# Optimization experiments

Measured on AMD Instinct MI355X. Metric: run time of the kernel, lower is better.

The kernel has to match this reference:

```python
import jax, jax.numpy as jnp
import numpy as np

NEG_SLOPE = 0.2  # PyG GATConv default negative_slope


def gat_conv(h_in, src, dst, W, a_src, a_dst, bias, concat):
    """PyG GATConv: linear -> per-edge attention -> segment softmax -> scatter-add.
    h_in: [N, Fin]; W: [heads*C, Fin]; a_src/a_dst: [heads, C]; bias: [heads*C] or [C].
    add_self_loops=True (PyG default)."""
    N = h_in.shape[0]
    heads, C = a_src.shape
    loop = jnp.arange(N, dtype=src.dtype)
    s = jnp.concatenate([src, loop])
    d = jnp.concatenate([dst, loop])
    h = (h_in @ W.T).reshape(N, heads, C)          # [N, H, C]
    al_s = (h * a_src).sum(-1)                      # [N, H]
    al_d = (h * a_dst).sum(-1)                      # [N, H]
    e = jax.nn.leaky_relu(al_s[s] + al_d[d], NEG_SLOPE)  # [E, H]
    emax = jax.ops.segment_max(e, d, num_segments=N)     # every node has a self loop
    ex = jnp.exp(e - emax[d])
    denom = jax.ops.segment_sum(ex, d, num_segments=N)
    alpha = ex / denom[d]                           # [E, H]
    msg = alpha[:, :, None] * h[s]                  # [E, H, C]
    out = jax.ops.segment_sum(msg, d, num_segments=N)    # [N, H, C]
    if concat:
        out = out.reshape(N, heads * C)
    else:
        out = out.mean(axis=1)
    return out + bias


def setup_inputs() -> dict:
    key = jax.random.key(0)
    ks = jax.random.split(key, 14)
    B, N, T = 1, 20000, 4
    E = 320000
    HID, HEADS, OUT = 64, 4, 64
    sc = 0.1
    x = jax.random.normal(ks[0], (B, N, T), dtype=jnp.float32)
    edge_index = jax.random.randint(ks[1], (2, E), 0, N, dtype=jnp.int64)
    time_idx = jnp.arange(T, dtype=jnp.float32).reshape(T, 1)
    return {
        "x": x,
        "edge_index": edge_index,
        "time_idx": time_idx,
        "Wt": jax.random.normal(ks[2], (HID, 1), jnp.float32) * sc,
        "bt": jnp.zeros((HID,), jnp.float32),
        "Wf": jax.random.normal(ks[3], (HID, 1), jnp.float32) * sc,
        "bf": jnp.zeros((HID,), jnp.float32),
        "W1": jax.random.normal(ks[4], (HEADS * HID, HID), jnp.float32) * sc,
        "a_src1": jax.random.normal(ks[5], (HEADS, HID), jnp.float32) * sc,
        "a_dst1": jax.random.normal(ks[6], (HEADS, HID), jnp.float32) * sc,
        "b1": jnp.zeros((HEADS * HID,), jnp.float32),
        "temporal_attention": jnp.ones((T,), jnp.float32),
        "W2": jax.random.normal(ks[7], (OUT, HEADS * HID), jnp.float32) * sc,
        "a_src2": jax.random.normal(ks[8], (1, OUT), jnp.float32) * sc,
        "a_dst2": jax.random.normal(ks[9], (1, OUT), jnp.float32) * sc,
        "b2": jnp.zeros((OUT,), jnp.float32),
    }


def reference(x, edge_index, time_idx, Wt, bt, Wf, bf, W1, a_src1, a_dst1, b1,
              temporal_attention, W2, a_src2, a_dst2, b2):
    B, N, T = x.shape  # features dim == time_steps
    src, dst = edge_index[0], edge_index[1]
    time_emb = time_idx @ Wt.T + bt                 # [T, hidden]
    tw = jax.nn.softmax(temporal_attention)         # [T]
    combined = jnp.zeros((B * N, a_src1.shape[0] * a_src1.shape[1]), x.dtype)
    for t in range(T):  # small static time loop, as in original
        feats = x[:, :, t].reshape(-1, 1)           # [B*N, 1]
        emb = feats @ Wf.T + bf + time_emb[t]       # [B*N, hidden]
        h = gat_conv(emb, src, dst, W1, a_src1, a_dst1, b1, concat=True)
        combined = combined + tw[t] * jax.nn.relu(h)  # dropout is identity in eval
    out = gat_conv(combined, src, dst, W2, a_src2, a_dst2, b2, concat=False)
    return out.reshape(B, N, -1)
```

## Files before the change

kernel.cpp:

```cpp
#include <hip/hip_runtime.h>
#include <hip/hip_bf16.h>

#define NEG 0.2f
#define NELL 64

#define P_U   0
#define P_W   256
#define P_PS  1280
#define P_PD  1284
#define P_QS  1288
#define P_QD  1304
#define P_TW  1320
#define P_WT  1324
#define P_CNT 2560

typedef __bf16 bf16x8 __attribute__((ext_vector_type(8)));
typedef float  f32x4  __attribute__((ext_vector_type(4)));

__device__ __forceinline__ float lrelu(float v){ return v > 0.f ? v : NEG*v; }
__device__ __forceinline__ unsigned short f2bf(float f){
    unsigned u = __float_as_uint(f);
    unsigned r = u + 0x7fffu + ((u >> 16) & 1u);
    return (unsigned short)(r >> 16);
}
__device__ __forceinline__ float bflo(unsigned u){ return __uint_as_float(u << 16); }
__device__ __forceinline__ float bfhi(unsigned u){ return __uint_as_float(u & 0xffff0000u); }

__global__ void zeroK(int* deg, int N){
    int i = blockIdx.x*256 + threadIdx.x;
    if (i < N) deg[i] = 0;
}

__global__ void ellpreK(const int* ei, int E, int* deg, int* ell,
                        const float* time_idx, const float* Wt, const float* bt,
                        const float* Wf, const float* bf, const float* W1,
                        const float* as1, const float* ad1, const float* b1,
                        const float* ta, const float* W2,
                        float* P, unsigned short* W2bf, int EB)
{
    int tid = threadIdx.x, bid = blockIdx.x;
    if (bid < EB){
        int e = bid*256 + tid;
        if (e < E){
            int d = ei[E+e];
            int pos = atomicAdd(&deg[d], 1);
            if (pos < NELL) ell[d*NELL + pos] = ei[e];
        }
        return;
    }
    if (bid > EB){
        int i0 = (bid - EB - 1)*256 + tid;
        for (int i = i0; i < 16384; i += 40*256) W2bf[i] = f2bf(W2[i]);
        return;
    }
    __shared__ float Zl[5][64];
    if (tid < 64){
        float wtk = Wt[tid], btk = bt[tid], bfk = bf[tid];
        Zl[0][tid] = Wf[tid];
        #pragma unroll
        for (int t = 0; t < 4; ++t)
            Zl[1+t][tid] = bfk + time_idx[t]*wtk + btk;
    }
    __syncthreads();
    {
        const float* wrow = W1 + tid*64;
        float uu = 0.f, v0 = 0.f, v1 = 0.f, v2 = 0.f, v3 = 0.f;
        for (int k = 0; k < 64; k += 4){
            float4 w4 = *reinterpret_cast<const float4*>(wrow + k);
            uu += w4.x*Zl[0][k] + w4.y*Zl[0][k+1] + w4.z*Zl[0][k+2] + w4.w*Zl[0][k+3];
            v0 += w4.x*Zl[1][k] + w4.y*Zl[1][k+1] + w4.z*Zl[1][k+2] + w4.w*Zl[1][k+3];
            v1 += w4.x*Zl[2][k] + w4.y*Zl[2][k+1] + w4.z*Zl[2][k+2] + w4.w*Zl[2][k+3];
            v2 += w4.x*Zl[3][k] + w4.y*Zl[3][k+1] + w4.z*Zl[3][k+2] + w4.w*Zl[3][k+3];
            v3 += w4.x*Zl[4][k] + w4.y*Zl[4][k+1] + w4.z*Zl[4][k+2] + w4.w*Zl[4][k+3];
        }
        float b = b1[tid];
        P[P_U + tid] = uu;
        P[P_W + 0*256 + tid] = v0 + b;
        P[P_W + 1*256 + tid] = v1 + b;
        P[P_W + 2*256 + tid] = v2 + b;
        P[P_W + 3*256 + tid] = v3 + b;
    }
    __syncthreads();
    if (tid < 4){
        int h = tid; float ps = 0.f, pd = 0.f;
        for (int c = 0; c < 64; ++c){
            float uv = P[P_U + h*64 + c];
            ps += uv * as1[h*64+c];
            pd += uv * ad1[h*64+c];
        }
        P[P_PS+h] = ps; P[P_PD+h] = pd;
    }
    if (tid < 16){
        int t = tid >> 2, h = tid & 3;
        float qs = 0.f, qd = 0.f;
        for (int c = 0; c < 64; ++c){
            float v = P[P_W + t*256 + h*64 + c] - b1[h*64+c];
            qs += v * as1[h*64+c];
            qd += v * ad1[h*64+c];
        }
        P[P_QS + t*4 + h] = qs;
        P[P_QD + t*4 + h] = qd;
    }
    if (tid == 0){
        float m = ta[0];
        for (int t = 1; t < 4; ++t) m = fmaxf(m, ta[t]);
        float s = 0.f, e[4];
        for (int t = 0; t < 4; ++t){ e[t] = __expf(ta[t]-m); s += e[t]; }
        for (int t = 0; t < 4; ++t) P[P_TW+t] = e[t]/s;
    }
    __syncthreads();
    for (int idx = tid; idx < 1024; idx += 256){
        int c = idx >> 2, t = idx & 3;
        P[P_WT + idx] = P[P_W + t*256 + c];
    }
}

__launch_bounds__(256)
__global__ void gat1h2K(const float* x, const int* deg, const int* ell,
                        const float* P, const unsigned short* W2bfg,
                        const float* as2, const float* ad2,
                        unsigned short* h2bf, float* als2, float* ald2, int N)
{
    __shared__ unsigned short Abf[64*264];
    __shared__ float4 Sl[64][4];
    __shared__ float  Ul[256];
    __shared__ float4 WTl[256];
    __shared__ float  Pl[44];
    int tid = threadIdx.x;
    Ul[tid] = P[P_U + tid];
    WTl[tid] = reinterpret_cast<const float4*>(P + P_WT)[tid];
    if (tid < 44) Pl[tid] = P[P_PS + tid];
    __syncthreads();

    int nl = tid >> 2, t = tid & 3;
    int n  = blockIdx.x*64 + nl;
    {
        float s_out[4] = {0.f,0.f,0.f,0.f};
        if (n < N){
            float xn = x[n*4 + t];
            float ps[4], qsum[4], den[4], num[4];
            #pragma unroll
            for (int h = 0; h < 4; ++h){
                ps[h]   = Pl[h];
                qsum[h] = Pl[8 + t*4 + h] + xn*Pl[4 + h] + Pl[24 + t*4 + h];
                float ex = __expf(lrelu(xn*ps[h] + qsum[h]));
                den[h] = ex; num[h] = ex*xn;
            }
            int dgn = min(deg[n], NELL);
            const int* row = ell + n*NELL;
            int j = 0;
            for (; j + 4 <= dgn; j += 4){
                float v0 = x[row[j]*4 + t];
                float v1 = x[row[j+1]*4 + t];
                float v2 = x[row[j+2]*4 + t];
                float v3 = x[row[j+3]*4 + t];
                #pragma unroll
                for (int h = 0; h < 4; ++h){
                    float e0 = __expf(lrelu(v0*ps[h] + qsum[h]));
                    float e1 = __expf(lrelu(v1*ps[h] + qsum[h]));
                    float e2 = __expf(lrelu(v2*ps[h] + qsum[h]));
                    float e3 = __expf(lrelu(v3*ps[h] + qsum[h]));
                    den[h] += (e0 + e1) + (e2 + e3);
                    num[h] += e0*v0 + e1*v1 + e2*v2 + e3*v3;
                }
            }
            for (; j < dgn; ++j){
                float v = x[row[j]*4 + t];
                #pragma unroll
                for (int h = 0; h < 4; ++h){
                    float ex = __expf(lrelu(v*ps[h] + qsum[h]));
                    den[h] += ex; num[h] += ex*v;
                }
            }
            #pragma unroll
            for (int h = 0; h < 4; ++h) s_out[h] = num[h]/den[h];
        }
        #pragma unroll
        for (int h = 0; h < 4; ++h)
            reinterpret_cast<float*>(&Sl[nl][h])[t] = s_out[h];
    }
    __syncthreads();

    {
        float tw0 = Pl[40], tw1 = Pl[41], tw2 = Pl[42], tw3 = Pl[43];
        int q = t;
        float4 s4 = Sl[nl][q];
        unsigned int* arow = reinterpret_cast<unsigned int*>(&Abf[nl*264 + q*64]);
        #pragma unroll 8
        for (int jj = 0; jj < 64; jj += 2){
            int c = q*64 + jj;
            float4 wa = WTl[c], wb = WTl[c+1];
            float ua = Ul[c], ub = Ul[c+1];
            float v0 = tw0*fmaxf(s4.x*ua + wa.x, 0.f) + tw1*fmaxf(s4.y*ua + wa.y, 0.f)
                     + tw2*fmaxf(s4.z*ua + wa.z, 0.f) + tw3*fmaxf(s4.w*ua + wa.w, 0.f);
            float v1 = tw0*fmaxf(s4.x*ub + wb.x, 0.f) + tw1*fmaxf(s4.y*ub + wb.y, 0.f)
                     + tw2*fmaxf(s4.z*ub + wb.z, 0.f) + tw3*fmaxf(s4.w*ub + wb.w, 0.f);
            arow[jj>>1] = (unsigned)f2bf(v0) | ((unsigned)f2bf(v1) << 16);
        }
    }
    __syncthreads();

    int w = tid >> 6, lane = tid & 63, lr = lane & 15, lhi = lane >> 4;
    int r0 = w*16;
    bf16x8 a[8];
    #pragma unroll
    for (int kk = 0; kk < 8; ++kk)
        a[kk] = *reinterpret_cast<const bf16x8*>(&Abf[(r0+lr)*264 + kk*32 + lhi*8]);
    float s1[4] = {0.f,0.f,0.f,0.f}, s2[4] = {0.f,0.f,0.f,0.f};
    int gbase = blockIdx.x*64 + r0 + lhi*4;
    #pragma unroll
    for (int nt = 0; nt < 4; ++nt){
        f32x4 acc = {0.f,0.f,0.f,0.f};
        const unsigned short* bp = W2bfg + (nt*16 + lr)*256 + lhi*8;
        #pragma unroll
        for (int kk = 0; kk < 8; ++kk){
            bf16x8 b = *reinterpret_cast<const bf16x8*>(bp + kk*32);
            acc = __builtin_amdgcn_mfma_f32_16x16x32_bf16(a[kk], b, acc, 0, 0, 0);
        }
        float oas = as2[nt*16 + lr], oad = ad2[nt*16 + lr];
        #pragma unroll
        for (int r = 0; r < 4; ++r){
            int g = gbase + r;
            if (g < N) h2bf[(size_t)g*64 + nt*16 + lr] = f2bf(acc[r]);
            s1[r] += acc[r]*oas;
            s2[r] += acc[r]*oad;
        }
    }
    #pragma unroll
    for (int r = 0; r < 4; ++r){
        float v1 = s1[r], v2 = s2[r];
        #pragma unroll
        for (int off = 8; off > 0; off >>= 1){
            v1 += __shfl_xor(v1, off);
            v2 += __shfl_xor(v2, off);
        }
        int g = gbase + r;
        if (lr == 0 && g < N){ als2[g] = v1; ald2[g] = v2; }
    }
}

__launch_bounds__(256)
__global__ void attnpvK(const unsigned short* h2bf, const float* als2, const float* ald2,
                        const int* deg, const int* ell, const float* b2,
                        float* out, int N)
{
    __shared__ int   sbuf[8][32];
    __shared__ float wbuf[8][32];
    int hw = threadIdx.x >> 5, lane = threadIdx.x & 31;
    int n = blockIdx.x*8 + hw;
    if (n >= N) return;
    float aldn = ald2[n];
    int dgn = min(deg[n], NELL);
    const int* row = ell + n*NELL;
    float sw = __expf(lrelu(als2[n] + aldn));
    float den = sw;
    unsigned us = reinterpret_cast<const unsigned*>(h2bf + ((size_t)n<<6))[lane];
    float acc0 = sw * bflo(us);
    float acc1 = sw * bfhi(us);
    for (int base = 0; base < dgn; base += 32){
        int cnt = min(32, dgn - base);
        int j = base + lane;
        int s = 0; float ex = 0.f;
        if (j < dgn){ s = row[j]; ex = __expf(lrelu(als2[s] + aldn)); }
        sbuf[hw][lane] = s; wbuf[hw][lane] = ex;
        float sx = ex;
        #pragma unroll
        for (int off = 16; off; off >>= 1) sx += __shfl_xor(sx, off);
        den += sx;
        int i = 0;
        for (; i + 4 <= cnt; i += 4){
            int   s0 = sbuf[hw][i],   s1 = sbuf[hw][i+1], s2 = sbuf[hw][i+2], s3 = sbuf[hw][i+3];
            float w0 = wbuf[hw][i],   w1 = wbuf[hw][i+1], w2 = wbuf[hw][i+2], w3 = wbuf[hw][i+3];
            unsigned g0 = reinterpret_cast<const unsigned*>(h2bf + ((size_t)s0<<6))[lane];
            unsigned g1 = reinterpret_cast<const unsigned*>(h2bf + ((size_t)s1<<6))[lane];
            unsigned g2 = reinterpret_cast<const unsigned*>(h2bf + ((size_t)s2<<6))[lane];
            unsigned g3 = reinterpret_cast<const unsigned*>(h2bf + ((size_t)s3<<6))[lane];
            acc0 += w0*bflo(g0); acc1 += w0*bfhi(g0);
            acc0 += w1*bflo(g1); acc1 += w1*bfhi(g1);
            acc0 += w2*bflo(g2); acc1 += w2*bfhi(g2);
            acc0 += w3*bflo(g3); acc1 += w3*bfhi(g3);
        }
        for (; i < cnt; ++i){
            float wv = wbuf[hw][i];
            unsigned g = reinterpret_cast<const unsigned*>(h2bf + ((size_t)sbuf[hw][i]<<6))[lane];
            acc0 += wv*bflo(g); acc1 += wv*bfhi(g);
        }
    }
    float rd = 1.f/den;
    int c = lane*2;
    float2 o;
    o.x = acc0*rd + b2[c];
    o.y = acc1*rd + b2[c+1];
    reinterpret_cast<float2*>(out + (size_t)n*64)[lane] = o;
}

extern "C" void kernel_launch(void* const* d_in, const int* in_sizes, int n_in,
                              void* d_out, int out_size, void* d_ws, size_t ws_size,
                              hipStream_t stream)
{
    const float* x        = (const float*)d_in[0];
    const int*   ei       = (const int*)  d_in[1];
    const float* time_idx = (const float*)d_in[2];
    const float* Wt       = (const float*)d_in[3];
    const float* bt       = (const float*)d_in[4];
    const float* Wf       = (const float*)d_in[5];
    const float* bf       = (const float*)d_in[6];
    const float* W1       = (const float*)d_in[7];
    const float* as1      = (const float*)d_in[8];
    const float* ad1      = (const float*)d_in[9];
    const float* b1       = (const float*)d_in[10];
    const float* ta       = (const float*)d_in[11];
    const float* W2       = (const float*)d_in[12];
    const float* as2      = (const float*)d_in[13];
    const float* ad2      = (const float*)d_in[14];
    const float* b2       = (const float*)d_in[15];

    int N = in_sizes[0] / 4;
    int E = in_sizes[1] / 2;

    char* w = (char*)d_ws;
    auto al = [](size_t v){ return (v + 255) & ~(size_t)255; };
    size_t off = 0;
    float* P     = (float*)(w + off); off = al(off + P_CNT*sizeof(float));
    unsigned short* W2bf = (unsigned short*)(w + off); off = al(off + 16384*sizeof(unsigned short));
    int*   deg   = (int*)  (w + off); off = al(off + (size_t)N*sizeof(int));
    int*   ell   = (int*)  (w + off); off = al(off + (size_t)N*NELL*sizeof(int));
    unsigned short* h2bf = (unsigned short*)(w + off); off = al(off + (size_t)N*64*sizeof(unsigned short));
    float* als2  = (float*)(w + off); off = al(off + (size_t)N*sizeof(float));
    float* ald2  = (float*)(w + off); off = al(off + (size_t)N*sizeof(float));
    (void)off; (void)ws_size; (void)n_in; (void)out_size;

    int EB = (E + 255)/256;

    zeroK<<<(N + 255)/256, 256, 0, stream>>>(deg, N);
    ellpreK<<<EB + 41, 256, 0, stream>>>(ei, E, deg, ell,
                                         time_idx, Wt, bt, Wf, bf, W1, as1, ad1, b1, ta, W2,
                                         P, W2bf, EB);
    gat1h2K<<<(N + 63)/64, 256, 0, stream>>>(x, deg, ell, P, W2bf, as2, ad2, h2bf, als2, ald2, N);
    attnpvK<<<(N + 7)/8, 256, 0, stream>>>(h2bf, als2, ald2, deg, ell, b2, (float*)d_out, N);
}
```

Measured before the change: 65.53 us.

## Halve nodes per block in gat1h2K, split edge loop across thread pairs

```diff
diff --git a/kernel.cpp b/kernel.cpp
--- a/kernel.cpp
+++ b/kernel.cpp
@@ -3,6 +3,7 @@
 
 #define NEG 0.2f
 #define NELL 64
+#define GT 32
 
 #define P_U   0
 #define P_W   256
@@ -121,21 +122,24 @@
                         const float* as2, const float* ad2,
                         unsigned short* h2bf, float* als2, float* ald2, int N)
 {
-    __shared__ unsigned short Abf[64*264];
-    __shared__ float4 Sl[64][4];
+    __shared__ unsigned short Abf[GT*264];
+    __shared__ float  Slf[GT][4][4];
     __shared__ float  Ul[256];
     __shared__ float4 WTl[256];
     __shared__ float  Pl[44];
+    __shared__ float  redL[2][2][GT];
     int tid = threadIdx.x;
     Ul[tid] = P[P_U + tid];
     WTl[tid] = reinterpret_cast<const float4*>(P + P_WT)[tid];
     if (tid < 44) Pl[tid] = P[P_PS + tid];
     __syncthreads();
 
-    int nl = tid >> 2, t = tid & 3;
-    int n  = blockIdx.x*64 + nl;
+    int nl = tid >> 3, sub = tid & 7, t = sub >> 1, half = sub & 1;
+    int n0 = blockIdx.x*GT;
+    int n  = n0 + nl;
+
     {
-        float s_out[4] = {0.f,0.f,0.f,0.f};
+        float o[4] = {0.f,0.f,0.f,0.f};
         if (n < N){
             float xn = x[n*4 + t];
             float ps[4], qsum[4], den[4], num[4];
@@ -143,17 +147,17 @@
             for (int h = 0; h < 4; ++h){
                 ps[h]   = Pl[h];
                 qsum[h] = Pl[8 + t*4 + h] + xn*Pl[4 + h] + Pl[24 + t*4 + h];
-                float ex = __expf(lrelu(xn*ps[h] + qsum[h]));
-                den[h] = ex; num[h] = ex*xn;
+                if (half == 0){
+                    float ex = __expf(lrelu(xn*ps[h] + qsum[h]));
+                    den[h] = ex; num[h] = ex*xn;
+                } else { den[h] = 0.f; num[h] = 0.f; }
             }
             int dgn = min(deg[n], NELL);
             const int* row = ell + n*NELL;
-            int j = 0;
-            for (; j + 4 <= dgn; j += 4){
-                float v0 = x[row[j]*4 + t];
-                float v1 = x[row[j+1]*4 + t];
-                float v2 = x[row[j+2]*4 + t];
-                float v3 = x[row[j+3]*4 + t];
+            int j = half;
+            for (; j + 6 < dgn; j += 8){
+                int s0 = row[j], s1 = row[j+2], s2 = row[j+4], s3 = row[j+6];
+                float v0 = x[s0*4 + t], v1 = x[s1*4 + t], v2 = x[s2*4 + t], v3 = x[s3*4 + t];
                 #pragma unroll
                 for (int h = 0; h < 4; ++h){
                     float e0 = __expf(lrelu(v0*ps[h] + qsum[h]));
@@ -164,7 +168,7 @@
                     num[h] += e0*v0 + e1*v1 + e2*v2 + e3*v3;
                 }
             }
-            for (; j < dgn; ++j){
+            for (; j < dgn; j += 2){
                 float v = x[row[j]*4 + t];
                 #pragma unroll
                 for (int h = 0; h < 4; ++h){
@@ -173,69 +177,85 @@
                 }
             }
             #pragma unroll
-            for (int h = 0; h < 4; ++h) s_out[h] = num[h]/den[h];
-        }
-        #pragma unroll
-        for (int h = 0; h < 4; ++h)
-            reinterpret_cast<float*>(&Sl[nl][h])[t] = s_out[h];
+            for (int h = 0; h < 4; ++h){
+                float d = den[h] + __shfl_xor(den[h], 1);
+                float m = num[h] + __shfl_xor(num[h], 1);
+                o[h] = m/d;
+            }
+        }
+        if (half == 0){
+            #pragma unroll
+            for (int h = 0; h < 4; ++h) Slf[nl][h][t] = o[h];
+        }
     }
     __syncthreads();
 
     {
+        int q = sub, h = q >> 1;
         float tw0 = Pl[40], tw1 = Pl[41], tw2 = Pl[42], tw3 = Pl[43];
-        int q = t;
-        float4 s4 = Sl[nl][q];
-        unsigned int* arow = reinterpret_cast<unsigned int*>(&Abf[nl*264 + q*64]);
+        float sx = Slf[nl][h][0], sy = Slf[nl][h][1], sz = Slf[nl][h][2], sw = Slf[nl][h][3];
+        unsigned* arow = reinterpret_cast<unsigned*>(&Abf[nl*264 + q*32]);
         #pragma unroll 8
-        for (int jj = 0; jj < 64; jj += 2){
-            int c = q*64 + jj;
+        for (int jj = 0; jj < 32; jj += 2){
+            int c = q*32 + jj;
             float4 wa = WTl[c], wb = WTl[c+1];
             float ua = Ul[c], ub = Ul[c+1];
-            float v0 = tw0*fmaxf(s4.x*ua + wa.x, 0.f) + tw1*fmaxf(s4.y*ua + wa.y, 0.f)
-                     + tw2*fmaxf(s4.z*ua + wa.z, 0.f) + tw3*fmaxf(s4.w*ua + wa.w, 0.f);
-            float v1 = tw0*fmaxf(s4.x*ub + wb.x, 0.f) + tw1*fmaxf(s4.y*ub + wb.y, 0.f)
-                     + tw2*fmaxf(s4.z*ub + wb.z, 0.f) + tw3*fmaxf(s4.w*ub + wb.w, 0.f);
+            float v0 = tw0*fmaxf(sx*ua + wa.x, 0.f) + tw1*fmaxf(sy*ua + wa.y, 0.f)
+                     + tw2*fmaxf(sz*ua + wa.z, 0.f) + tw3*fmaxf(sw*ua + wa.w, 0.f);
+            float v1 = tw0*fmaxf(sx*ub + wb.x, 0.f) + tw1*fmaxf(sy*ub + wb.y, 0.f)
+                     + tw2*fmaxf(sz*ub + wb.z, 0.f) + tw3*fmaxf(sw*ub + wb.w, 0.f);
             arow[jj>>1] = (unsigned)f2bf(v0) | ((unsigned)f2bf(v1) << 16);
         }
     }
     __syncthreads();
 
-    int w = tid >> 6, lane = tid & 63, lr = lane & 15, lhi = lane >> 4;
-    int r0 = w*16;
-    bf16x8 a[8];
-    #pragma unroll
-    for (int kk = 0; kk < 8; ++kk)
-        a[kk] = *reinterpret_cast<const bf16x8*>(&Abf[(r0+lr)*264 + kk*32 + lhi*8]);
-    float s1[4] = {0.f,0.f,0.f,0.f}, s2[4] = {0.f,0.f,0.f,0.f};
-    int gbase = blockIdx.x*64 + r0 + lhi*4;
-    #pragma unroll
-    for (int nt = 0; nt < 4; ++nt){
-        f32x4 acc = {0.f,0.f,0.f,0.f};
-        const unsigned short* bp = W2bfg + (nt*16 + lr)*256 + lhi*8;
-        #pragma unroll
-        for (int kk = 0; kk < 8; ++kk){
-            bf16x8 b = *reinterpret_cast<const bf16x8*>(bp + kk*32);
-            acc = __builtin_amdgcn_mfma_f32_16x16x32_bf16(a[kk], b, acc, 0, 0, 0);
-        }
-        float oas = as2[nt*16 + lr], oad = ad2[nt*16 + lr];
+    {
+        int w = tid >> 6, lane = tid & 63, lr = lane & 15, lhi = lane >> 4;
+        int rg = w & 1, cg = w >> 1;
+        bf16x8 a[8];
+        #pragma unroll
+        for (int kk = 0; kk < 8; ++kk)
+            a[kk] = *reinterpret_cast<const bf16x8*>(&Abf[(rg*16 + lr)*264 + kk*32 + lhi*8]);
+        float s1[4] = {0.f,0.f,0.f,0.f}, s2[4] = {0.f,0.f,0.f,0.f};
+        int gbase = n0 + rg*16 + lhi*4;
+        #pragma unroll
+        for (int nt2 = 0; nt2 < 2; ++nt2){
+            int nt = cg*2 + nt2;
+            f32x4 acc = {0.f,0.f,0.f,0.f};
+            const unsigned short* bp = W2bfg + (nt*16 + lr)*256 + lhi*8;
+            #pragma unroll
+            for (int kk = 0; kk < 8; ++kk){
+                bf16x8 b = *reinterpret_cast<const bf16x8*>(bp + kk*32);
+                acc = __builtin_amdgcn_mfma_f32_16x16x32_bf16(a[kk], b, acc, 0, 0, 0);
+            }
+            int o = nt*16 + lr;
+            float oas = as2[o], oad = ad2[o];
+            #pragma unroll
+            for (int r = 0; r < 4; ++r){
+                int g = gbase + r;
+                if (g < N) h2bf[(size_t)g*64 + o] = f2bf(acc[r]);
+                s1[r] += acc[r]*oas;
+                s2[r] += acc[r]*oad;
+            }
+        }
         #pragma unroll
         for (int r = 0; r < 4; ++r){
-            int g = gbase + r;
-            if (g < N) h2bf[(size_t)g*64 + nt*16 + lr] = f2bf(acc[r]);
-            s1[r] += acc[r]*oas;
-            s2[r] += acc[r]*oad;
-        }
-    }
-    #pragma unroll
-    for (int r = 0; r < 4; ++r){
-        float v1 = s1[r], v2 = s2[r];
-        #pragma unroll
-        for (int off = 8; off > 0; off >>= 1){
-            v1 += __shfl_xor(v1, off);
-            v2 += __shfl_xor(v2, off);
-        }
-        int g = gbase + r;
-        if (lr == 0 && g < N){ als2[g] = v1; ald2[g] = v2; }
+            float v1 = s1[r], v2 = s2[r];
+            #pragma unroll
+            for (int off = 8; off > 0; off >>= 1){
+                v1 += __shfl_xor(v1, off);
+                v2 += __shfl_xor(v2, off);
+            }
+            if (lr == 0){
+                redL[0][cg][rg*16 + lhi*4 + r] = v1;
+                redL[1][cg][rg*16 + lhi*4 + r] = v2;
+            }
+        }
+    }
+    __syncthreads();
+    if (tid < GT && n0 + tid < N){
+        als2[n0 + tid] = redL[0][0][tid] + redL[0][1][tid];
+        ald2[n0 + tid] = redL[1][0][tid] + redL[1][1][tid];
     }
 }
 
@@ -336,6 +356,6 @@
     ellpreK<<<EB + 41, 256, 0, stream>>>(ei, E, deg, ell,
                                          time_idx, Wt, bt, Wf, bf, W1, as1, ad1, b1, ta, W2,
                                          P, W2bf, EB);
-    gat1h2K<<<(N + 63)/64, 256, 0, stream>>>(x, deg, ell, P, W2bf, as2, ad2, h2bf, als2, ald2, N);
+    gat1h2K<<<(N + GT - 1)/GT, 256, 0, stream>>>(x, deg, ell, P, W2bf, as2, ad2, h2bf, als2, ald2, N);
     attnpvK<<<(N + 7)/8, 256, 0, stream>>>(h2bf, als2, ald2, deg, ell, b2, (float*)d_out, N);
 }
```

After: 63.68 us. 2.8% less time.
